# Performance work log

Hardware: AMD Instinct MI355X
Metric: run time of the kernel (lower is better)

## Reference

```python
import jax, jax.numpy as jnp
import numpy as np

HID = 192
EPS = 1e-5

def _bn(x, g, b):
    # BatchNorm1d, training mode: batch stats over all leading axes, biased var
    ax = tuple(range(x.ndim - 1))
    m = x.mean(axis=ax)
    v = x.var(axis=ax)
    return (x - m) * jax.lax.rsqrt(v + EPS) * g + b

def _glorot(k, shape):
    lim = np.sqrt(6.0 / (shape[0] + shape[1]))
    return jax.random.uniform(k, shape, jnp.float32, -lim, lim)

def setup_inputs() -> dict:
    key = jax.random.key(0)
    ks = jax.random.split(key, 8)
    B, N, F, C = 16, 1024, 128, 10
    x = jax.random.normal(ks[0], (B, N, F), jnp.float32)
    adj = (jax.random.uniform(ks[1], (B, N, N)) < 0.01).astype(jnp.float32)
    adj = jnp.maximum(adj, jnp.swapaxes(adj, 1, 2))
    return dict(
        x=x, adj=adj,
        bn_feat_g=jnp.ones((F,), jnp.float32), bn_feat_b=jnp.full((F,), 1e-4, jnp.float32),
        W_feat=_glorot(ks[2], (F, HID)),
        bns_conv_g=jnp.ones((3, HID), jnp.float32), bns_conv_b=jnp.full((3, HID), 1e-4, jnp.float32),
        convs_W=jnp.stack([_glorot(jax.random.fold_in(ks[3], i), (HID, HID)) for i in range(3)]),
        convs_b=jnp.zeros((3, HID), jnp.float32),
        bn_fc_g=jnp.ones((HID,), jnp.float32), bn_fc_b=jnp.full((HID,), 1e-4, jnp.float32),
        lin_W=_glorot(ks[4], (HID, HID)), lin_b=jnp.zeros((HID,), jnp.float32),
        bn_hid_g=jnp.ones((HID,), jnp.float32), bn_hid_b=jnp.full((HID,), 1e-4, jnp.float32),
        cls_W=_glorot(ks[5], (HID, 10)), cls_b=jnp.zeros((10,), jnp.float32),
    )

def reference(x, adj, bn_feat_g, bn_feat_b, W_feat, bns_conv_g, bns_conv_b,
              convs_W, convs_b, bn_fc_g, bn_fc_b, lin_W, lin_b,
              bn_hid_g, bn_hid_b, cls_W, cls_b):
    B, N, _ = x.shape
    # dense_to_sparse discards edge values -> binary edges; add remaining self loops (weight 1)
    A = (adj != 0).astype(x.dtype)
    A = jnp.maximum(A, jnp.eye(N, dtype=x.dtype))
    deg = A.sum(-1)                                   # [B,N]
    dis = jnp.where(deg > 0, deg ** -0.5, 0.0)
    A_hat = dis[:, :, None] * A * dis[:, None, :]      # D^-1/2 (A+I) D^-1/2
    h = _bn(x, bn_feat_g, bn_feat_b)
    # conv_feat has gfn=True: pure linear transform, no bias, no propagation
    h = jax.nn.relu(jnp.einsum('bnf,fh->bnh', h, W_feat))
    for i in range(convs_W.shape[0]):
        h = _bn(h, bns_conv_g[i], bns_conv_b[i])
        h = jax.nn.relu(jnp.einsum('bij,bjh->bih', A_hat, h @ convs_W[i]) + convs_b[i])
    g = h.mean(axis=1)                                 # global_mean_pool -> [B,HID]
    g = _bn(g, bn_fc_g, bn_fc_b)
    g = jax.nn.relu(g @ lin_W + lin_b)
    g = _bn(g, bn_hid_g, bn_hid_b)
    logits = g @ cls_W + cls_b
    return jax.nn.log_softmax(logits, axis=-1)
```

## Files before the change

kernel.cpp:

```cpp
#include <hip/hip_runtime.h>
#include <hip/hip_bf16.h>

#define BB 16
#define NN 1024
#define FF 128
#define HH 192
#define NROWS (BB*NN)
#define MAXC 128
#define EPSV 1e-5f

constexpr size_t OFF_H0  = 0;
constexpr size_t OFF_ZB  = OFF_H0 + (size_t)NROWS*HH/2;
constexpr size_t OFF_WPF = OFF_ZB + (size_t)NROWS*HH/2;
constexpr size_t OFF_WPC = OFF_WPF + (size_t)HH*FF/2;
constexpr size_t OFF_BF  = OFF_WPC + (size_t)HH*HH/2;
constexpr size_t OFF_BC  = OFF_BF + HH;
constexpr size_t OFF_DIS = OFF_BC + HH;
constexpr size_t OFF_G   = OFF_DIS + NROWS;
constexpr size_t OFF_ST  = OFF_G + BB*HH;
constexpr size_t ST_SIZE = 512 + 3*8*512;
constexpr size_t OFF_FLAG= OFF_ST + ST_SIZE;
constexpr size_t OFF_CNT = OFF_FLAG + 1;
constexpr size_t OFF_COLS= OFF_CNT + NROWS;

typedef __attribute__((ext_vector_type(8))) short short8;
typedef __attribute__((ext_vector_type(4))) float f32x4;
typedef __attribute__((ext_vector_type(4))) unsigned int u32x4;
typedef __attribute__((ext_vector_type(2))) unsigned int u32x2;

static __device__ __forceinline__ float bf(const __hip_bfloat16 v) {
    return __bfloat162float(v);
}
static __device__ __forceinline__ float ldin(const void* p, size_t i, int isf) {
    return isf ? ((const float*)p)[i]
               : __bfloat162float(((const __hip_bfloat16*)p)[i]);
}
static __host__ __device__ __forceinline__ float* stage_h(float* ws, int s ) {
    return ws + OFF_ST + 512 + (size_t)s*8*512;
}
static __device__ __forceinline__ float blo(unsigned int u) {
    union { unsigned int x; float f; } v; v.x = u << 16; return v.f;
}
static __device__ __forceinline__ float bhi(unsigned int u) {
    union { unsigned int x; float f; } v; v.x = u & 0xFFFF0000u; return v.f;
}
static __device__ __forceinline__ unsigned int packbf(float a, float b) {
    union { unsigned int u; __hip_bfloat16 h[2]; } p;
    p.h[0] = __float2bfloat16(a); p.h[1] = __float2bfloat16(b);
    return p.u;
}

__global__ void detect_and_zero(const unsigned int* __restrict__ adjw, float* ws) {
    __shared__ int evid;
    int tid = threadIdx.x;
    if (tid == 0) evid = 0;
    __syncthreads();
    int local = 0;
    for (int k = tid; k < 16384; k += 256) {
        unsigned int w = adjw[k];
        if ((w & 0xFFFFu) == 0x3F80u) local++;
    }
    if (local) atomicAdd(&evid, local);
    for (size_t k = tid; k < ST_SIZE; k += 256) ws[OFF_ST + k] = 0.f;
    for (int k = tid; k < BB*HH; k += 256) ws[OFF_G + k] = 0.f;
    __syncthreads();
    if (tid == 0) ((int*)ws)[OFF_FLAG] = (evid == 0) ? 1 : 0;
}

__global__ __launch_bounds__(256) void phase1(const void* __restrict__ adj,
                                              const void* __restrict__ x, float* ws) {
    const int isf = ((const int*)ws)[OFF_FLAG];
    int tid = threadIdx.x;
    if (blockIdx.x < NROWS) {
        int row = blockIdx.x;
        int i   = row & (NN - 1);
        __shared__ int cnt_s;
        __shared__ unsigned short colbuf[MAXC];
        if (tid == 0) cnt_s = 0;
        __syncthreads();
        int j0 = tid*4;
        unsigned int bits[4];
        if (isf) {
            u32x4 v = *(const u32x4*)((const unsigned int*)adj + (size_t)row*NN + j0);
            bits[0]=v[0]; bits[1]=v[1]; bits[2]=v[2]; bits[3]=v[3];
        } else {
            u32x2 v = *(const u32x2*)((const unsigned short*)adj + (size_t)row*NN + j0);
            bits[0]=(v[0]&0xFFFFu); bits[1]=(v[0]>>16); bits[2]=(v[1]&0xFFFFu); bits[3]=(v[1]>>16);
        }
        #pragma unroll
        for (int e = 0; e < 4; ++e) {
            int j = j0 + e;
            if ((bits[e] << 1) != 0u || j == i) {
                int p = atomicAdd(&cnt_s, 1);
                if (p < MAXC) colbuf[p] = (unsigned short)j;
            }
        }
        __syncthreads();
        int c = cnt_s; if (c > MAXC) c = MAXC;
        if (tid == 0) {
            ((int*)(ws + OFF_CNT))[row] = c;
            ws[OFF_DIS + row] = rsqrtf((float)cnt_s);
        }
        unsigned short* cols = (unsigned short*)(ws + OFF_COLS);
        for (int k = tid; k < c; k += 256) cols[(size_t)row*MAXC + k] = colbuf[k];
    } else {
        int b2 = blockIdx.x - NROWS;
        int f = tid & (FF-1), half = tid >> 7;
        int r0 = b2*64 + half*32;
        float s = 0.f, sq = 0.f;
        for (int r = 0; r < 32; ++r) {
            float v = ldin(x, (size_t)(r0 + r)*FF + f, isf);
            s += v; sq += v*v;
        }
        atomicAdd(&ws[OFF_ST + f], s);
        atomicAdd(&ws[OFF_ST + 256 + f], sq);
    }
}

__global__ void prep_feat(const void* __restrict__ W_feat,
                          const void* __restrict__ gg, const void* __restrict__ bb,
                          float* ws) {
    const int isf = ((const int*)ws)[OFF_FLAG];
    int n = blockIdx.x, k = threadIdx.x;
    const float* st = ws + OFF_ST;
    float m   = st[k] * (1.f/NROWS);
    float var = st[256+k] * (1.f/NROWS) - m*m;
    float a   = ldin(gg, k, isf) * rsqrtf(var + EPSV);
    float c   = ldin(bb, k, isf) - m*a;
    float wv  = ldin(W_feat, (size_t)k*HH + n, isf);
    ((__hip_bfloat16*)(ws + OFF_WPF))[(size_t)n*FF + k] = __float2bfloat16(a*wv);
    __shared__ float red[FF];
    red[k] = c*wv;
    __syncthreads();
    for (int s = FF/2; s > 0; s >>= 1) {
        if (k < s) red[k] += red[k + s];
        __syncthreads();
    }
    if (k == 0) ws[OFF_BF + n] = red[0];
}

__global__ void prep_conv(const void* __restrict__ convs_W,
                          const void* __restrict__ gg, const void* __restrict__ bb,
                          int layer, float* ws) {
    const int isf = ((const int*)ws)[OFF_FLAG];
    int n = blockIdx.x, k = threadIdx.x;
    const float* st = stage_h(ws, layer);
    float s = 0.f, sq = 0.f;
    #pragma unroll
    for (int bkt = 0; bkt < 8; ++bkt) {
        s  += st[bkt*512 + k];
        sq += st[bkt*512 + 256 + k];
    }
    float m   = s * (1.f/NROWS);
    float var = sq * (1.f/NROWS) - m*m;
    float a   = ldin(gg, (size_t)layer*HH + k, isf) * rsqrtf(var + EPSV);
    float c   = ldin(bb, (size_t)layer*HH + k, isf) - m*a;
    float wv  = ldin(convs_W, (size_t)layer*HH*HH + (size_t)k*HH + n, isf);
    ((__hip_bfloat16*)(ws + OFF_WPC))[(size_t)n*HH + k] = __float2bfloat16(a*wv);
    __shared__ float red[HH];
    red[k] = c*wv;
    __syncthreads();
    if (k < 96) red[k] += red[k + 96];
    __syncthreads();
    for (int s2 = 48; s2 >= 3; s2 >>= 1) {
        if (k < s2) red[k] += red[k + s2];
        __syncthreads();
    }
    if (k == 0) ws[OFF_BC + n] = red[0] + red[1] + red[2];
}

template<int K, int MODE>
__global__ __launch_bounds__(256) void gemm_mfma(const void* __restrict__ A,
                                                 const __hip_bfloat16* __restrict__ BT,
                                                 const float* __restrict__ bias,
                                                 float* __restrict__ ws) {
    const int isf = ((const int*)ws)[OFF_FLAG];
    int lane = threadIdx.x & 63, w = threadIdx.x >> 6;
    int wr = w & 1, wc = w >> 1;
    int bi = blockIdx.x;
    int batch = bi & 15, seg = bi >> 4;
    int row0 = batch*NN + seg*32 + wr*16;
    int col0 = wc*96;
    int m    = lane & 15, quad = lane >> 4;
    f32x4 acc[6];
    #pragma unroll
    for (int t = 0; t < 6; ++t) acc[t] = f32x4{0.f,0.f,0.f,0.f};
    float bv[6];
    #pragma unroll
    for (int t = 0; t < 6; ++t) bv[t] = bias[col0 + t*16 + m];
    #pragma unroll
    for (int kb = 0; kb < K/32; ++kb) {
        short8 a;
        if (MODE == 0 && isf) {
            const float* Ar = (const float*)A + (size_t)(row0+m)*K + kb*32 + quad*8;
            f32x4 v0 = *(const f32x4*)Ar;
            f32x4 v1 = *(const f32x4*)(Ar + 4);
            union { short8 s8; __hip_bfloat16 h[8]; } u;
            #pragma unroll
            for (int e = 0; e < 4; ++e) {
                u.h[e]   = __float2bfloat16(v0[e]);
                u.h[e+4] = __float2bfloat16(v1[e]);
            }
            a = u.s8;
        } else {
            a = *(const short8*)((const __hip_bfloat16*)A +
                                 (size_t)(row0+m)*K + kb*32 + quad*8);
        }
        #pragma unroll
        for (int t = 0; t < 6; ++t) {
            short8 b = *(const short8*)(BT + (size_t)(col0 + t*16+m)*K + kb*32 + quad*8);
            acc[t] = __builtin_amdgcn_mfma_f32_16x16x32_bf16(a, b, acc[t], 0, 0, 0);
        }
    }
    if (MODE == 0) {
        __shared__ float sh[2*HH];
        for (int i = threadIdx.x; i < 2*HH; i += 256) sh[i] = 0.f;
        __syncthreads();
        __hip_bfloat16* H0 = (__hip_bfloat16*)(ws + OFF_H0);
        #pragma unroll
        for (int t = 0; t < 6; ++t) {
            int ch = col0 + t*16 + m;
            float s = 0.f, sq = 0.f;
            #pragma unroll
            for (int r = 0; r < 4; ++r) {
                float o = fmaxf(acc[t][r] + bv[t], 0.f);
                H0[(size_t)(row0 + quad*4 + r)*HH + ch] = __float2bfloat16(o);
                s += o; sq += o*o;
            }
            atomicAdd(&sh[ch], s);
            atomicAdd(&sh[HH + ch], sq);
        }
        __syncthreads();
        float* st = stage_h(ws, 0) + (bi & 7)*512;
        if (threadIdx.x < HH) {
            atomicAdd(&st[threadIdx.x], sh[threadIdx.x]);
            atomicAdd(&st[256 + threadIdx.x], sh[HH + threadIdx.x]);
        }
    } else {
        const float* dis = ws + OFF_DIS;
        __hip_bfloat16* Z = (__hip_bfloat16*)(ws + OFF_ZB);
        float sc[4];
        #pragma unroll
        for (int r = 0; r < 4; ++r) sc[r] = dis[row0 + quad*4 + r];
        #pragma unroll
        for (int t = 0; t < 6; ++t)
            #pragma unroll
            for (int r = 0; r < 4; ++r)
                Z[(size_t)(row0 + quad*4 + r)*HH + col0 + t*16 + m] =
                    __float2bfloat16((acc[t][r] + bv[t]) * sc[r]);
    }
}

__global__ __launch_bounds__(512) void spmm(const void* __restrict__ bias, int layer,
                                            float* __restrict__ stat_out, int is_pool,
                                            float* ws) {
    __shared__ unsigned int Zs[NN*16];
    const int isf = ((const int*)ws)[OFF_FLAG];
    int tid = threadIdx.x;
    int bi = blockIdx.x;
    int batch = bi & 15;
    int rest  = bi >> 4;
    int slice = rest % 6;
    int half  = rest / 6;
    int c0 = slice*32;
    const unsigned int* Zu = (const unsigned int*)(ws + OFF_ZB)
                             + (size_t)batch*NN*96 + c0/2;
    for (int i = tid; i < NN*16; i += 512) {
        int r = i >> 4, u = i & 15;
        Zs[i] = Zu[(size_t)r*96 + u];
    }
    __syncthreads();
    int d = tid & 7, rslot = tid >> 3;
    const float* dis = ws + OFF_DIS;
    const int* cnt = (const int*)(ws + OFF_CNT);
    const unsigned short* cols = (const unsigned short*)(ws + OFF_COLS);
    unsigned int* H0u = (unsigned int*)(ws + OFF_H0);
    float bch[4];
    #pragma unroll
    for (int e = 0; e < 4; ++e)
        bch[e] = ldin(bias, (size_t)layer*HH + c0 + d*4 + e, isf);
    float s_acc[4] = {0.f,0.f,0.f,0.f}, q_acc[4] = {0.f,0.f,0.f,0.f};
    for (int it = 0; it < 8; ++it) {
        int row = batch*NN + half*512 + it*64 + rslot;
        int c = cnt[row];
        const unsigned short* cl = cols + (size_t)row*MAXC;
        float a0=0.f, a1=0.f, a2=0.f, a3=0.f;
        int k = 0;
        for (; k + 8 <= c; k += 8) {
            u32x4 cw = *(const u32x4*)(cl + k);
            int j[8];
            j[0]=(int)(cw[0]&0xFFFFu); j[1]=(int)(cw[0]>>16);
            j[2]=(int)(cw[1]&0xFFFFu); j[3]=(int)(cw[1]>>16);
            j[4]=(int)(cw[2]&0xFFFFu); j[5]=(int)(cw[2]>>16);
            j[6]=(int)(cw[3]&0xFFFFu); j[7]=(int)(cw[3]>>16);
            u32x2 z[8];
            #pragma unroll
            for (int e = 0; e < 8; ++e)
                z[e] = *(const u32x2*)(&Zs[j[e]*16 + d*2]);
            #pragma unroll
            for (int e = 0; e < 8; ++e) {
                a0 += blo(z[e][0]); a1 += bhi(z[e][0]);
                a2 += blo(z[e][1]); a3 += bhi(z[e][1]);
            }
        }
        for (; k < c; ++k) {
            u32x2 z = *(const u32x2*)(&Zs[(int)cl[k]*16 + d*2]);
            a0 += blo(z[0]); a1 += bhi(z[0]);
            a2 += blo(z[1]); a3 += bhi(z[1]);
        }
        float dd = dis[row];
        float o0 = fmaxf(dd*a0 + bch[0], 0.f);
        float o1 = fmaxf(dd*a1 + bch[1], 0.f);
        float o2 = fmaxf(dd*a2 + bch[2], 0.f);
        float o3 = fmaxf(dd*a3 + bch[3], 0.f);
        u32x2 outw; outw[0] = packbf(o0,o1); outw[1] = packbf(o2,o3);
        *(u32x2*)(&H0u[(size_t)row*96 + c0/2 + d*2]) = outw;
        s_acc[0]+=o0; s_acc[1]+=o1; s_acc[2]+=o2; s_acc[3]+=o3;
        q_acc[0]+=o0*o0; q_acc[1]+=o1*o1; q_acc[2]+=o2*o2; q_acc[3]+=o3*o3;
    }
    #pragma unroll
    for (int e = 0; e < 4; ++e) {
        #pragma unroll
        for (int mask = 8; mask < 64; mask <<= 1) {
            s_acc[e] += __shfl_xor(s_acc[e], mask, 64);
            q_acc[e] += __shfl_xor(q_acc[e], mask, 64);
        }
    }
    if ((tid & 63) < 8) {
        if (is_pool) {
            #pragma unroll
            for (int e = 0; e < 4; ++e)
                atomicAdd(&ws[OFF_G + (size_t)batch*HH + c0 + d*4 + e], s_acc[e]);
        } else {
            float* st = stat_out + (bi & 7)*512;
            #pragma unroll
            for (int e = 0; e < 4; ++e) {
                atomicAdd(&st[c0 + d*4 + e],       s_acc[e]);
                atomicAdd(&st[256 + c0 + d*4 + e], q_acc[e]);
            }
        }
    }
}

__global__ __launch_bounds__(768) void tail(
                     const void* __restrict__ fc_g,  const void* __restrict__ fc_b,
                     const void* __restrict__ lin_W, const void* __restrict__ lin_b,
                     const void* __restrict__ hid_g, const void* __restrict__ hid_b,
                     const void* __restrict__ cls_W, const void* __restrict__ cls_b,
                     void* __restrict__ out, const float* ws) {
    __shared__ float g1[BB][HH];
    __shared__ float g2[BB][HH];
    __shared__ __hip_bfloat16 Wl[HH*HH];
    __shared__ float logits[BB][10];
    __shared__ float lse[BB];
    int tid = threadIdx.x;
    const int isf = ((const int*)ws)[OFF_FLAG];
    const float* g = ws + OFF_G;
    if (isf) {
        const float* Wp = (const float*)lin_W;
        for (int i = tid; i < HH*HH; i += 768) Wl[i] = __float2bfloat16(Wp[i]);
    } else {
        const __hip_bfloat16* Wp = (const __hip_bfloat16*)lin_W;
        for (int i = tid; i < HH*HH; i += 768) Wl[i] = Wp[i];
    }
    if (tid < HH) {
        float s = 0.f, sq = 0.f;
        for (int b = 0; b < BB; ++b) {
            float v = g[b*HH + tid] * (1.f/NN);
            s += v; sq += v*v;
        }
        float m = s*(1.f/BB), var = sq*(1.f/BB) - m*m;
        float a = ldin(fc_g, tid, isf) * rsqrtf(var + EPSV);
        float c = ldin(fc_b, tid, isf) - m*a;
        for (int b = 0; b < BB; ++b) g1[b][tid] = g[b*HH + tid]*(1.f/NN)*a + c;
    }
    __syncthreads();
    {
        int n = tid % HH, bg = tid / HH;
        float lb = ldin(lin_b, n, isf);
        float a0 = lb, a1 = lb, a2 = lb, a3 = lb;
        int b0 = bg*4;
        for (int k = 0; k < HH; ++k) {
            float wv = bf(Wl[k*HH + n]);
            a0 += g1[b0+0][k]*wv;
            a1 += g1[b0+1][k]*wv;
            a2 += g1[b0+2][k]*wv;
            a3 += g1[b0+3][k]*wv;
        }
        g2[b0+0][n] = fmaxf(a0, 0.f);
        g2[b0+1][n] = fmaxf(a1, 0.f);
        g2[b0+2][n] = fmaxf(a2, 0.f);
        g2[b0+3][n] = fmaxf(a3, 0.f);
    }
    __syncthreads();
    if (tid < HH) {
        float s = 0.f, sq = 0.f;
        for (int b = 0; b < BB; ++b) { float v = g2[b][tid]; s += v; sq += v*v; }
        float m = s*(1.f/BB), var = sq*(1.f/BB) - m*m;
        float a = ldin(hid_g, tid, isf) * rsqrtf(var + EPSV);
        float c = ldin(hid_b, tid, isf) - m*a;
        for (int b = 0; b < BB; ++b) g2[b][tid] = g2[b][tid]*a + c;
    }
    __syncthreads();
    if (tid < BB*10) {
        int b = tid/10, k = tid%10;
        float acc = ldin(cls_b, k, isf);
        for (int h = 0; h < HH; ++h) acc += g2[b][h] * ldin(cls_W, (size_t)h*10 + k, isf);
        logits[b][k] = acc;
    }
    __syncthreads();
    if (tid < BB) {
        float m = -1e30f;
        for (int k = 0; k < 10; ++k) m = fmaxf(m, logits[tid][k]);
        float s = 0.f;
        for (int k = 0; k < 10; ++k) s += expf(logits[tid][k] - m);
        lse[tid] = m + logf(s);
    }
    __syncthreads();
    if (tid < BB*10) {
        int b = tid/10;
        float v = logits[b][tid%10] - lse[b];
        if (isf) ((float*)out)[tid] = v;
        else     ((__hip_bfloat16*)out)[tid] = __float2bfloat16(v);
    }
}

extern "C" void kernel_launch(void* const* d_in, const int* in_sizes, int n_in,
                              void* d_out, int out_size, void* d_ws, size_t ws_size,
                              hipStream_t stream) {
    const void* x       = d_in[0];
    const void* adj     = d_in[1];
    const void* bnf_g   = d_in[2];
    const void* bnf_b   = d_in[3];
    const void* W_feat  = d_in[4];
    const void* bnc_g   = d_in[5];
    const void* bnc_b   = d_in[6];
    const void* convs_W = d_in[7];
    const void* convs_b = d_in[8];
    const void* fc_g    = d_in[9];
    const void* fc_b    = d_in[10];
    const void* lin_W   = d_in[11];
    const void* lin_b   = d_in[12];
    const void* hid_g   = d_in[13];
    const void* hid_b   = d_in[14];
    const void* cls_W   = d_in[15];
    const void* cls_b   = d_in[16];

    float* ws = (float*)d_ws;
    const __hip_bfloat16* WPF = (const __hip_bfloat16*)(ws + OFF_WPF);
    const __hip_bfloat16* WPC = (const __hip_bfloat16*)(ws + OFF_WPC);

    detect_and_zero<<<1, 256, 0, stream>>>((const unsigned int*)adj, ws);
    phase1<<<NROWS + 256, 256, 0, stream>>>(adj, x, ws);
    prep_feat<<<HH, FF, 0, stream>>>(W_feat, bnf_g, bnf_b, ws);
    gemm_mfma<FF, 0><<<NROWS/32, 256, 0, stream>>>(x, WPF, ws + OFF_BF, ws);
    for (int l = 0; l < 3; ++l) {
        prep_conv<<<HH, HH, 0, stream>>>(convs_W, bnc_g, bnc_b, l, ws);
        gemm_mfma<HH, 1><<<NROWS/32, 256, 0, stream>>>(
            (const void*)(ws + OFF_H0), WPC, ws + OFF_BC, ws);
        spmm<<<192, 512, 0, stream>>>(convs_b, l,
            (l < 2) ? stage_h(ws, l + 1) : nullptr, (l == 2) ? 1 : 0, ws);
    }
    tail<<<1, 768, 0, stream>>>(fc_g, fc_b, lin_W, lin_b,
                                hid_g, hid_b, cls_W, cls_b, d_out, ws);
}
```

Measured before the change: 331.7 us.

## Fold BatchNorm weight preparation into each GEMM block, dropping prep kernels

Removes the separate prep_feat and prep_conv launches. Each gemm_mfma block now computes the BatchNorm scale and shift, builds the scaled transposed weight in shared memory, and computes the folded bias itself. This saves four kernel launches and the global round trip for the prepared weights. In exchange, every block repeats the weight preparation, including a serial K-length bias dot product, and uses much more LDS, which can reduce occupancy.

```diff
diff --git a/kernel.cpp b/kernel.cpp
--- a/kernel.cpp
+++ b/kernel.cpp
@@ -11,11 +11,7 @@
 
 constexpr size_t OFF_H0  = 0;
 constexpr size_t OFF_ZB  = OFF_H0 + (size_t)NROWS*HH/2;
-constexpr size_t OFF_WPF = OFF_ZB + (size_t)NROWS*HH/2;
-constexpr size_t OFF_WPC = OFF_WPF + (size_t)HH*FF/2;
-constexpr size_t OFF_BF  = OFF_WPC + (size_t)HH*HH/2;
-constexpr size_t OFF_BC  = OFF_BF + HH;
-constexpr size_t OFF_DIS = OFF_BC + HH;
+constexpr size_t OFF_DIS = OFF_ZB + (size_t)NROWS*HH/2;
 constexpr size_t OFF_G   = OFF_DIS + NROWS;
 constexpr size_t OFF_ST  = OFF_G + BB*HH;
 constexpr size_t ST_SIZE = 512 + 3*8*512;
@@ -117,65 +113,53 @@
     }
 }
 
-__global__ void prep_feat(const void* __restrict__ W_feat,
-                          const void* __restrict__ gg, const void* __restrict__ bb,
-                          float* ws) {
-    const int isf = ((const int*)ws)[OFF_FLAG];
-    int n = blockIdx.x, k = threadIdx.x;
-    const float* st = ws + OFF_ST;
-    float m   = st[k] * (1.f/NROWS);
-    float var = st[256+k] * (1.f/NROWS) - m*m;
-    float a   = ldin(gg, k, isf) * rsqrtf(var + EPSV);
-    float c   = ldin(bb, k, isf) - m*a;
-    float wv  = ldin(W_feat, (size_t)k*HH + n, isf);
-    ((__hip_bfloat16*)(ws + OFF_WPF))[(size_t)n*FF + k] = __float2bfloat16(a*wv);
-    __shared__ float red[FF];
-    red[k] = c*wv;
-    __syncthreads();
-    for (int s = FF/2; s > 0; s >>= 1) {
-        if (k < s) red[k] += red[k + s];
-        __syncthreads();
-    }
-    if (k == 0) ws[OFF_BF + n] = red[0];
-}
-
-__global__ void prep_conv(const void* __restrict__ convs_W,
-                          const void* __restrict__ gg, const void* __restrict__ bb,
-                          int layer, float* ws) {
-    const int isf = ((const int*)ws)[OFF_FLAG];
-    int n = blockIdx.x, k = threadIdx.x;
-    const float* st = stage_h(ws, layer);
-    float s = 0.f, sq = 0.f;
-    #pragma unroll
-    for (int bkt = 0; bkt < 8; ++bkt) {
-        s  += st[bkt*512 + k];
-        sq += st[bkt*512 + 256 + k];
-    }
-    float m   = s * (1.f/NROWS);
-    float var = sq * (1.f/NROWS) - m*m;
-    float a   = ldin(gg, (size_t)layer*HH + k, isf) * rsqrtf(var + EPSV);
-    float c   = ldin(bb, (size_t)layer*HH + k, isf) - m*a;
-    float wv  = ldin(convs_W, (size_t)layer*HH*HH + (size_t)k*HH + n, isf);
-    ((__hip_bfloat16*)(ws + OFF_WPC))[(size_t)n*HH + k] = __float2bfloat16(a*wv);
-    __shared__ float red[HH];
-    red[k] = c*wv;
-    __syncthreads();
-    if (k < 96) red[k] += red[k + 96];
-    __syncthreads();
-    for (int s2 = 48; s2 >= 3; s2 >>= 1) {
-        if (k < s2) red[k] += red[k + s2];
-        __syncthreads();
-    }
-    if (k == 0) ws[OFF_BC + n] = red[0] + red[1] + red[2];
-}
-
 template<int K, int MODE>
 __global__ __launch_bounds__(256) void gemm_mfma(const void* __restrict__ A,
-                                                 const __hip_bfloat16* __restrict__ BT,
-                                                 const float* __restrict__ bias,
+                                                 const void* __restrict__ W_src,
+                                                 const void* __restrict__ g_src,
+                                                 const void* __restrict__ b_src,
+                                                 int layer,
                                                  float* __restrict__ ws) {
+    constexpr int KP = K + 8;
+    __shared__ __hip_bfloat16 BTs[HH*KP];
+    __shared__ float afold[K], cfold[K];
+    __shared__ float biasS[HH];
+    __shared__ float sh[2*HH];
     const int isf = ((const int*)ws)[OFF_FLAG];
-    int lane = threadIdx.x & 63, w = threadIdx.x >> 6;
+    int tid = threadIdx.x;
+
+    if (tid < K) {
+        float s, q;
+        if (MODE == 0) {
+            s = ws[OFF_ST + tid];
+            q = ws[OFF_ST + 256 + tid];
+        } else {
+            const float* st = stage_h(ws, layer);
+            s = 0.f; q = 0.f;
+            #pragma unroll
+            for (int b = 0; b < 8; ++b) { s += st[b*512 + tid]; q += st[b*512 + 256 + tid]; }
+        }
+        float m = s * (1.f/NROWS);
+        float var = q * (1.f/NROWS) - m*m;
+        float a = ldin(g_src, (size_t)layer*K + tid, isf) * rsqrtf(var + EPSV);
+        afold[tid] = a;
+        cfold[tid] = ldin(b_src, (size_t)layer*K + tid, isf) - m*a;
+    }
+    __syncthreads();
+    size_t w0 = (size_t)layer*K*HH;
+    if (tid < HH) {
+        float b = 0.f;
+        for (int k = 0; k < K; ++k)
+            b += cfold[k] * ldin(W_src, w0 + (size_t)k*HH + tid, isf);
+        biasS[tid] = b;
+    }
+    for (int idx = tid; idx < K*HH; idx += 256) {
+        int k = idx / HH, n = idx - k*HH;
+        BTs[n*KP + k] = __float2bfloat16(afold[k] * ldin(W_src, w0 + (size_t)idx, isf));
+    }
+    __syncthreads();
+
+    int lane = tid & 63, w = tid >> 6;
     int wr = w & 1, wc = w >> 1;
     int bi = blockIdx.x;
     int batch = bi & 15, seg = bi >> 4;
@@ -187,7 +171,7 @@
     for (int t = 0; t < 6; ++t) acc[t] = f32x4{0.f,0.f,0.f,0.f};
     float bv[6];
     #pragma unroll
-    for (int t = 0; t < 6; ++t) bv[t] = bias[col0 + t*16 + m];
+    for (int t = 0; t < 6; ++t) bv[t] = biasS[col0 + t*16 + m];
     #pragma unroll
     for (int kb = 0; kb < K/32; ++kb) {
         short8 a;
@@ -208,13 +192,12 @@
         }
         #pragma unroll
         for (int t = 0; t < 6; ++t) {
-            short8 b = *(const short8*)(BT + (size_t)(col0 + t*16+m)*K + kb*32 + quad*8);
+            short8 b = *(const short8*)(BTs + (size_t)(col0 + t*16 + m)*KP + kb*32 + quad*8);
             acc[t] = __builtin_amdgcn_mfma_f32_16x16x32_bf16(a, b, acc[t], 0, 0, 0);
         }
     }
     if (MODE == 0) {
-        __shared__ float sh[2*HH];
-        for (int i = threadIdx.x; i < 2*HH; i += 256) sh[i] = 0.f;
+        for (int i = tid; i < 2*HH; i += 256) sh[i] = 0.f;
         __syncthreads();
         __hip_bfloat16* H0 = (__hip_bfloat16*)(ws + OFF_H0);
         #pragma unroll
@@ -231,10 +214,10 @@
             atomicAdd(&sh[HH + ch], sq);
         }
         __syncthreads();
-        float* st = stage_h(ws, 0) + (bi & 7)*512;
-        if (threadIdx.x < HH) {
-            atomicAdd(&st[threadIdx.x], sh[threadIdx.x]);
-            atomicAdd(&st[256 + threadIdx.x], sh[HH + threadIdx.x]);
+        float* st = stage_h(ws, 0) + (size_t)(bi & 7)*512;
+        if (tid < HH) {
+            atomicAdd(&st[tid], sh[tid]);
+            atomicAdd(&st[256 + tid], sh[HH + tid]);
         }
     } else {
         const float* dis = ws + OFF_DIS;
@@ -447,17 +430,13 @@
     const void* cls_b   = d_in[16];
 
     float* ws = (float*)d_ws;
-    const __hip_bfloat16* WPF = (const __hip_bfloat16*)(ws + OFF_WPF);
-    const __hip_bfloat16* WPC = (const __hip_bfloat16*)(ws + OFF_WPC);
 
     detect_and_zero<<<1, 256, 0, stream>>>((const unsigned int*)adj, ws);
     phase1<<<NROWS + 256, 256, 0, stream>>>(adj, x, ws);
-    prep_feat<<<HH, FF, 0, stream>>>(W_feat, bnf_g, bnf_b, ws);
-    gemm_mfma<FF, 0><<<NROWS/32, 256, 0, stream>>>(x, WPF, ws + OFF_BF, ws);
+    gemm_mfma<FF, 0><<<NROWS/32, 256, 0, stream>>>(x, W_feat, bnf_g, bnf_b, 0, ws);
     for (int l = 0; l < 3; ++l) {
-        prep_conv<<<HH, HH, 0, stream>>>(convs_W, bnc_g, bnc_b, l, ws);
         gemm_mfma<HH, 1><<<NROWS/32, 256, 0, stream>>>(
-            (const void*)(ws + OFF_H0), WPC, ws + OFF_BC, ws);
+            (const void*)(ws + OFF_H0), convs_W, bnc_g, bnc_b, l, ws);
         spmm<<<192, 512, 0, stream>>>(convs_b, l,
             (l < 2) ? stage_h(ws, l + 1) : nullptr, (l == 2) ? 1 : 0, ws);
     }
```

Measured after the change: 426.9 us. 28.7% more time.

## Remove detect kernel, detect dtype per block, and split spmm into quarters

Applied to the files above, without the earlier changes.

Removes the single-block detect_and_zero launch. Each kernel now detects the input dtype locally from the first 1024 adjacency words, and phase1 zeroes the accumulators. Feature BN statistics are written as per-block partials and reduced in prep_feat instead of using global atomics. spmm now launches 384 blocks, each covering a quarter of a graph instead of a half, which adds parallelism but means every block reloads the full Z slice into shared memory. The cost is redundant detection reads in every block and a 256-entry serial loop in prep_feat.

```diff
diff --git a/kernel.cpp b/kernel.cpp
--- a/kernel.cpp
+++ b/kernel.cpp
@@ -11,16 +11,17 @@
 
 constexpr size_t OFF_H0  = 0;
 constexpr size_t OFF_ZB  = OFF_H0 + (size_t)NROWS*HH/2;
-constexpr size_t OFF_WPF = OFF_ZB + (size_t)NROWS*HH/2;
+constexpr size_t OFF_DIS = OFF_ZB + (size_t)NROWS*HH/2;
+constexpr size_t OFF_G   = OFF_DIS + NROWS;
+constexpr size_t OFF_SH  = OFF_G + BB*HH;
+constexpr size_t SH_SIZE = 3*8*512;
+constexpr size_t ZERO_SZ = BB*HH + SH_SIZE;
+constexpr size_t OFF_XB  = OFF_SH + SH_SIZE;
+constexpr size_t OFF_WPF = OFF_XB + 256*256;
 constexpr size_t OFF_WPC = OFF_WPF + (size_t)HH*FF/2;
 constexpr size_t OFF_BF  = OFF_WPC + (size_t)HH*HH/2;
 constexpr size_t OFF_BC  = OFF_BF + HH;
-constexpr size_t OFF_DIS = OFF_BC + HH;
-constexpr size_t OFF_G   = OFF_DIS + NROWS;
-constexpr size_t OFF_ST  = OFF_G + BB*HH;
-constexpr size_t ST_SIZE = 512 + 3*8*512;
-constexpr size_t OFF_FLAG= OFF_ST + ST_SIZE;
-constexpr size_t OFF_CNT = OFF_FLAG + 1;
+constexpr size_t OFF_CNT = OFF_BC + HH;
 constexpr size_t OFF_COLS= OFF_CNT + NROWS;
 
 typedef __attribute__((ext_vector_type(8))) short short8;
@@ -36,7 +37,7 @@
                : __bfloat162float(((const __hip_bfloat16*)p)[i]);
 }
 static __host__ __device__ __forceinline__ float* stage_h(float* ws, int s ) {
-    return ws + OFF_ST + 512 + (size_t)s*8*512;
+    return ws + OFF_SH + (size_t)s*8*512;
 }
 static __device__ __forceinline__ float blo(unsigned int u) {
     union { unsigned int x; float f; } v; v.x = u << 16; return v.f;
@@ -50,29 +51,31 @@
     return p.u;
 }
 
-__global__ void detect_and_zero(const unsigned int* __restrict__ adjw, float* ws) {
-    __shared__ int evid;
-    int tid = threadIdx.x;
-    if (tid == 0) evid = 0;
-    __syncthreads();
-    int local = 0;
-    for (int k = tid; k < 16384; k += 256) {
-        unsigned int w = adjw[k];
-        if ((w & 0xFFFFu) == 0x3F80u) local++;
-    }
-    if (local) atomicAdd(&evid, local);
-    for (size_t k = tid; k < ST_SIZE; k += 256) ws[OFF_ST + k] = 0.f;
-    for (int k = tid; k < BB*HH; k += 256) ws[OFF_G + k] = 0.f;
-    __syncthreads();
-    if (tid == 0) ((int*)ws)[OFF_FLAG] = (evid == 0) ? 1 : 0;
+template<int NTHR>
+static __device__ __forceinline__ int detect_isf(const unsigned int* __restrict__ adjw,
+                                                 int tid, int* sh_flag) {
+    if (tid == 0) *sh_flag = 0;
+    __syncthreads();
+    int hit = 0;
+    #pragma unroll
+    for (int k = tid; k < 1024; k += NTHR)
+        if ((adjw[k] & 0xFFFFu) == 0x3F80u) hit = 1;
+    if (hit) *sh_flag = 1;
+    __syncthreads();
+    return (*sh_flag == 0) ? 1 : 0;
 }
 
 __global__ __launch_bounds__(256) void phase1(const void* __restrict__ adj,
                                               const void* __restrict__ x, float* ws) {
-    const int isf = ((const int*)ws)[OFF_FLAG];
+    __shared__ int sflag;
     int tid = threadIdx.x;
+    const int isf = detect_isf<256>((const unsigned int*)adj, tid, &sflag);
     if (blockIdx.x < NROWS) {
         int row = blockIdx.x;
+        if (row < 60) {
+            size_t idx = (size_t)row*256 + tid;
+            if (idx < ZERO_SZ) ws[OFF_G + idx] = 0.f;
+        }
         int i   = row & (NN - 1);
         __shared__ int cnt_s;
         __shared__ unsigned short colbuf[MAXC];
@@ -112,19 +115,30 @@
             float v = ldin(x, (size_t)(r0 + r)*FF + f, isf);
             s += v; sq += v*v;
         }
-        atomicAdd(&ws[OFF_ST + f], s);
-        atomicAdd(&ws[OFF_ST + 256 + f], sq);
-    }
-}
-
-__global__ void prep_feat(const void* __restrict__ W_feat,
+        __shared__ float xs[256];
+        if (half == 1) { xs[f] = s; xs[128 + f] = sq; }
+        __syncthreads();
+        if (half == 0) {
+            ws[OFF_XB + (size_t)b2*256 + f]       = s  + xs[f];
+            ws[OFF_XB + (size_t)b2*256 + 128 + f] = sq + xs[128 + f];
+        }
+    }
+}
+
+__global__ __launch_bounds__(128) void prep_feat(const void* __restrict__ adj,
+                          const void* __restrict__ W_feat,
                           const void* __restrict__ gg, const void* __restrict__ bb,
                           float* ws) {
-    const int isf = ((const int*)ws)[OFF_FLAG];
+    __shared__ int sflag;
     int n = blockIdx.x, k = threadIdx.x;
-    const float* st = ws + OFF_ST;
-    float m   = st[k] * (1.f/NROWS);
-    float var = st[256+k] * (1.f/NROWS) - m*m;
+    const int isf = detect_isf<128>((const unsigned int*)adj, k, &sflag);
+    float s = 0.f, q = 0.f;
+    for (int b = 0; b < 256; ++b) {
+        s += ws[OFF_XB + (size_t)b*256 + k];
+        q += ws[OFF_XB + (size_t)b*256 + 128 + k];
+    }
+    float m   = s * (1.f/NROWS);
+    float var = q * (1.f/NROWS) - m*m;
     float a   = ldin(gg, k, isf) * rsqrtf(var + EPSV);
     float c   = ldin(bb, k, isf) - m*a;
     float wv  = ldin(W_feat, (size_t)k*HH + n, isf);
@@ -132,18 +146,20 @@
     __shared__ float red[FF];
     red[k] = c*wv;
     __syncthreads();
-    for (int s = FF/2; s > 0; s >>= 1) {
-        if (k < s) red[k] += red[k + s];
+    for (int s2 = FF/2; s2 > 0; s2 >>= 1) {
+        if (k < s2) red[k] += red[k + s2];
         __syncthreads();
     }
     if (k == 0) ws[OFF_BF + n] = red[0];
 }
 
-__global__ void prep_conv(const void* __restrict__ convs_W,
+__global__ __launch_bounds__(192) void prep_conv(const void* __restrict__ adj,
+                          const void* __restrict__ convs_W,
                           const void* __restrict__ gg, const void* __restrict__ bb,
                           int layer, float* ws) {
-    const int isf = ((const int*)ws)[OFF_FLAG];
+    __shared__ int sflag;
     int n = blockIdx.x, k = threadIdx.x;
+    const int isf = detect_isf<192>((const unsigned int*)adj, k, &sflag);
     const float* st = stage_h(ws, layer);
     float s = 0.f, sq = 0.f;
     #pragma unroll
@@ -170,12 +186,15 @@
 }
 
 template<int K, int MODE>
-__global__ __launch_bounds__(256) void gemm_mfma(const void* __restrict__ A,
+__global__ __launch_bounds__(256) void gemm_mfma(const void* __restrict__ adj,
+                                                 const void* __restrict__ A,
                                                  const __hip_bfloat16* __restrict__ BT,
                                                  const float* __restrict__ bias,
                                                  float* __restrict__ ws) {
-    const int isf = ((const int*)ws)[OFF_FLAG];
-    int lane = threadIdx.x & 63, w = threadIdx.x >> 6;
+    __shared__ int sflag;
+    int tid = threadIdx.x;
+    const int isf = detect_isf<256>((const unsigned int*)adj, tid, &sflag);
+    int lane = tid & 63, w = tid >> 6;
     int wr = w & 1, wc = w >> 1;
     int bi = blockIdx.x;
     int batch = bi & 15, seg = bi >> 4;
@@ -214,7 +233,7 @@
     }
     if (MODE == 0) {
         __shared__ float sh[2*HH];
-        for (int i = threadIdx.x; i < 2*HH; i += 256) sh[i] = 0.f;
+        for (int i = tid; i < 2*HH; i += 256) sh[i] = 0.f;
         __syncthreads();
         __hip_bfloat16* H0 = (__hip_bfloat16*)(ws + OFF_H0);
         #pragma unroll
@@ -231,10 +250,10 @@
             atomicAdd(&sh[HH + ch], sq);
         }
         __syncthreads();
-        float* st = stage_h(ws, 0) + (bi & 7)*512;
-        if (threadIdx.x < HH) {
-            atomicAdd(&st[threadIdx.x], sh[threadIdx.x]);
-            atomicAdd(&st[256 + threadIdx.x], sh[HH + threadIdx.x]);
+        float* st = stage_h(ws, 0) + (size_t)(bi & 7)*512;
+        if (tid < HH) {
+            atomicAdd(&st[tid], sh[tid]);
+            atomicAdd(&st[256 + tid], sh[HH + tid]);
         }
     } else {
         const float* dis = ws + OFF_DIS;
@@ -251,17 +270,19 @@
     }
 }
 
-__global__ __launch_bounds__(512) void spmm(const void* __restrict__ bias, int layer,
+__global__ __launch_bounds__(512) void spmm(const void* __restrict__ adj,
+                                            const void* __restrict__ bias, int layer,
                                             float* __restrict__ stat_out, int is_pool,
                                             float* ws) {
     __shared__ unsigned int Zs[NN*16];
-    const int isf = ((const int*)ws)[OFF_FLAG];
+    __shared__ int sflag;
     int tid = threadIdx.x;
+    const int isf = detect_isf<512>((const unsigned int*)adj, tid, &sflag);
     int bi = blockIdx.x;
     int batch = bi & 15;
     int rest  = bi >> 4;
     int slice = rest % 6;
-    int half  = rest / 6;
+    int qtr   = rest / 6;
     int c0 = slice*32;
     const unsigned int* Zu = (const unsigned int*)(ws + OFF_ZB)
                              + (size_t)batch*NN*96 + c0/2;
@@ -280,8 +301,8 @@
     for (int e = 0; e < 4; ++e)
         bch[e] = ldin(bias, (size_t)layer*HH + c0 + d*4 + e, isf);
     float s_acc[4] = {0.f,0.f,0.f,0.f}, q_acc[4] = {0.f,0.f,0.f,0.f};
-    for (int it = 0; it < 8; ++it) {
-        int row = batch*NN + half*512 + it*64 + rslot;
+    for (int it = 0; it < 4; ++it) {
+        int row = batch*NN + qtr*256 + it*64 + rslot;
         int c = cnt[row];
         const unsigned short* cl = cols + (size_t)row*MAXC;
         float a0=0.f, a1=0.f, a2=0.f, a3=0.f;
@@ -342,7 +363,7 @@
     }
 }
 
-__global__ __launch_bounds__(768) void tail(
+__global__ __launch_bounds__(768) void tail(const void* __restrict__ adj,
                      const void* __restrict__ fc_g,  const void* __restrict__ fc_b,
                      const void* __restrict__ lin_W, const void* __restrict__ lin_b,
                      const void* __restrict__ hid_g, const void* __restrict__ hid_b,
@@ -353,8 +374,9 @@
     __shared__ __hip_bfloat16 Wl[HH*HH];
     __shared__ float logits[BB][10];
     __shared__ float lse[BB];
+    __shared__ int sflag;
     int tid = threadIdx.x;
-    const int isf = ((const int*)ws)[OFF_FLAG];
+    const int isf = detect_isf<768>((const unsigned int*)adj, tid, &sflag);
     const float* g = ws + OFF_G;
     if (isf) {
         const float* Wp = (const float*)lin_W;
@@ -450,17 +472,16 @@
     const __hip_bfloat16* WPF = (const __hip_bfloat16*)(ws + OFF_WPF);
     const __hip_bfloat16* WPC = (const __hip_bfloat16*)(ws + OFF_WPC);
 
-    detect_and_zero<<<1, 256, 0, stream>>>((const unsigned int*)adj, ws);
     phase1<<<NROWS + 256, 256, 0, stream>>>(adj, x, ws);
-    prep_feat<<<HH, FF, 0, stream>>>(W_feat, bnf_g, bnf_b, ws);
-    gemm_mfma<FF, 0><<<NROWS/32, 256, 0, stream>>>(x, WPF, ws + OFF_BF, ws);
+    prep_feat<<<HH, FF, 0, stream>>>(adj, W_feat, bnf_g, bnf_b, ws);
+    gemm_mfma<FF, 0><<<NROWS/32, 256, 0, stream>>>(adj, x, WPF, ws + OFF_BF, ws);
     for (int l = 0; l < 3; ++l) {
-        prep_conv<<<HH, HH, 0, stream>>>(convs_W, bnc_g, bnc_b, l, ws);
+        prep_conv<<<HH, HH, 0, stream>>>(adj, convs_W, bnc_g, bnc_b, l, ws);
         gemm_mfma<HH, 1><<<NROWS/32, 256, 0, stream>>>(
-            (const void*)(ws + OFF_H0), WPC, ws + OFF_BC, ws);
-        spmm<<<192, 512, 0, stream>>>(convs_b, l,
+            adj, (const void*)(ws + OFF_H0), WPC, ws + OFF_BC, ws);
+        spmm<<<384, 512, 0, stream>>>(adj, convs_b, l,
             (l < 2) ? stage_h(ws, l + 1) : nullptr, (l == 2) ? 1 : 0, ws);
     }
-    tail<<<1, 768, 0, stream>>>(fc_g, fc_b, lin_W, lin_b,
+    tail<<<1, 768, 0, stream>>>(adj, fc_g, fc_b, lin_W, lin_b,
                                 hid_g, hid_b, cls_W, cls_b, d_out, ws);
 }
```

Result: faster. 315.9 us (-4.8%).
